# Performance work log

Hardware: AMD Instinct MI355X
Metric: run time of the kernel (lower is better)

The kernel has to match this reference:

```python
import jax, jax.numpy as jnp
import numpy as np

N_NODES = 50000
N_EDGES = 800000


def gcn_layer(h_in, W, b, src, dst, n_nodes):
    """PyG GCNConv: linear transform, add self-loops, symmetric-normalized scatter-add."""
    h = h_in @ W  # [N, out]
    loop = jnp.arange(n_nodes, dtype=src.dtype)
    s = jnp.concatenate([src, loop])  # [E+N]
    d = jnp.concatenate([dst, loop])  # [E+N]
    deg = jax.ops.segment_sum(jnp.ones_like(d, dtype=h.dtype), d, num_segments=n_nodes)
    dinv = jnp.where(deg > 0, jax.lax.rsqrt(deg), 0.0)  # deg^{-1/2}
    norm = dinv[s] * dinv[d]  # [E+N]
    msg = h[s] * norm[:, None]  # gather + scale, [E+N, out]
    out = jax.ops.segment_sum(msg, d, num_segments=n_nodes)  # scatter-add
    return out + b


def setup_inputs() -> dict:
    key = jax.random.key(0)
    ks = jax.random.split(key, 8)
    Din, H1, H2, Dout = 128, 128, 128, 64
    x = jax.random.normal(ks[0], (N_NODES, Din), dtype=jnp.float32)
    edge_index = jax.random.randint(ks[1], (2, N_EDGES), 0, N_NODES, dtype=jnp.int64)
    # Glorot-ish init for weights
    W1 = jax.random.normal(ks[2], (Din, H1), dtype=jnp.float32) / np.sqrt(Din)
    W2 = jax.random.normal(ks[3], (H1, H2), dtype=jnp.float32) / np.sqrt(H1)
    W3 = jax.random.normal(ks[4], (H2, Dout), dtype=jnp.float32) / np.sqrt(H2)
    b1 = jnp.zeros((H1,), dtype=jnp.float32)
    b2 = jnp.zeros((H2,), dtype=jnp.float32)
    b3 = jnp.zeros((Dout,), dtype=jnp.float32)
    return {"x": x, "edge_index": edge_index, "W1": W1, "b1": b1,
            "W2": W2, "b2": b2, "W3": W3, "b3": b3}


def reference(x, edge_index, W1, b1, W2, b2, W3, b3):
    src, dst = edge_index[0], edge_index[1]
    n = x.shape[0]
    h = gcn_layer(x, W1, b1, src, dst, n)
    h = jax.nn.relu(h)  # dropout p=0 -> identity
    h = gcn_layer(h, W2, b2, src, dst, n)
    h = jax.nn.relu(h)
    h = gcn_layer(h, W3, b3, src, dst, n)
    return h
```

## Files before the change

kernel.cpp:

```cpp
#include <hip/hip_runtime.h>
#include <hip/hip_fp16.h>

#define N_NODES 50000
#define N_EDGES 800000
#define CEILDIV(a,b) (((a)+(b)-1)/(b))
#define NB_SCAN CEILDIV(N_NODES, 256)

typedef _Float16 half8 __attribute__((ext_vector_type(8)));
typedef float    f32x4 __attribute__((ext_vector_type(4)));

__global__ __launch_bounds__(256) void k_deg_count(const int* __restrict__ dst,
                                                   int* __restrict__ degcnt, int e) {
    int i = blockIdx.x * 256 + threadIdx.x;
    if (i < e) atomicAdd(&degcnt[dst[i]], 1);
}

__global__ __launch_bounds__(256) void k_blocksum(const int* __restrict__ degcnt,
                                                  int* __restrict__ bsum, int n) {
    __shared__ int part[256];
    const int tid = threadIdx.x;
    const int gid = blockIdx.x * 256 + tid;
    part[tid] = (gid < n) ? degcnt[gid] : 0;
    __syncthreads();
    for (int off = 128; off > 0; off >>= 1) {
        if (tid < off) part[tid] += part[tid + off];
        __syncthreads();
    }
    if (tid == 0) bsum[blockIdx.x] = part[0];
}

__global__ __launch_bounds__(256) void k_scanb(const int* __restrict__ bsum,
                                               int* __restrict__ boff) {
    __shared__ int part[256];
    const int tid = threadIdx.x;
    part[tid] = (tid < NB_SCAN) ? bsum[tid] : 0;
    __syncthreads();
    for (int off = 1; off < 256; off <<= 1) {
        int v = (tid >= off) ? part[tid - off] : 0;
        __syncthreads();
        part[tid] += v;
        __syncthreads();
    }
    if (tid < NB_SCAN) boff[tid] = (tid == 0) ? 0 : part[tid - 1];
}

__global__ __launch_bounds__(256) void k_rowstart(const int* __restrict__ degcnt,
                                                  const int* __restrict__ boff,
                                                  int* __restrict__ rowstart,
                                                  float* __restrict__ dinv, int n) {
    __shared__ int part[256];
    const int tid = threadIdx.x;
    const int gid = blockIdx.x * 256 + tid;
    const int d = (gid < n) ? degcnt[gid] : 0;
    part[tid] = d;
    __syncthreads();
    for (int off = 1; off < 256; off <<= 1) {
        int v = (tid >= off) ? part[tid - off] : 0;
        __syncthreads();
        part[tid] += v;
        __syncthreads();
    }
    if (gid < n) {
        rowstart[gid] = boff[blockIdx.x] + part[tid] - d;
        dinv[gid] = rsqrtf((float)(d + 1));
    }
    if (gid == 0) rowstart[n] = N_EDGES;
}

__global__ __launch_bounds__(256) void k_bin(const int* __restrict__ src,
                                             const int* __restrict__ dst,
                                             const int* __restrict__ rowstart,
                                             int* __restrict__ cursor,
                                             int* __restrict__ esrc, int e) {
    int i = blockIdx.x * 256 + threadIdx.x;
    if (i < e) {
        int d = dst[i];
        int pos = rowstart[d] + atomicAdd(&cursor[d], 1);
        esrc[pos] = src[i];
    }
}

__global__ __launch_bounds__(256) void k_x2h(const float* __restrict__ x,
                                             __half* __restrict__ xh, long total) {
    long i = (long)(blockIdx.x * 256 + threadIdx.x) * 8;
    if (i >= total) return;
    float4 lo = ((const float4*)x)[i / 4];
    float4 hi = ((const float4*)x)[i / 4 + 1];
    union { __half2 h2[4]; uint4 u; } pk;
    pk.h2[0] = __floats2half2_rn(lo.x, lo.y);
    pk.h2[1] = __floats2half2_rn(lo.z, lo.w);
    pk.h2[2] = __floats2half2_rn(hi.x, hi.y);
    pk.h2[3] = __floats2half2_rn(hi.z, hi.w);
    ((uint4*)xh)[i / 8] = pk.u;
}

template<int KOUT>
__global__ __launch_bounds__(256) void k_w2h(const float* __restrict__ W,
                                             __half* __restrict__ Wt) {
    int idx = blockIdx.x * 256 + threadIdx.x;
    if (idx >= KOUT * 128) return;
    int c = idx >> 7;
    int k = idx & 127;
    Wt[c * 128 + k] = __float2half(W[(size_t)k * KOUT + c]);
}

template<int KOUT, bool RELU>
__global__ __launch_bounds__(256) void k_gemm(const __half* __restrict__ A,
                                              const __half* __restrict__ Wt,
                                              const float* __restrict__ dinv,
                                              __half* __restrict__ C, int n) {
    constexpr int NT     = KOUT / 16;
    constexpr int ABYTES = 64 * 256;
    constexpr int WBYTES = KOUT * 256;
    __shared__ uint4 ldsbuf[(ABYTES + WBYTES) / 16];
    char* Als = (char*)ldsbuf;
    char* Wls = Als + ABYTES;

    const int tid  = threadIdx.x;
    const int row0 = blockIdx.x * 64;

#pragma unroll
    for (int i = 0; i < 4; ++i) {
        int g   = tid + i * 256;
        int r   = g >> 4;
        int ch  = g & 15;
        int gr  = row0 + r;
        uint4 v = make_uint4(0u, 0u, 0u, 0u);
        if (gr < n) v = ((const uint4*)A)[(size_t)gr * 16 + ch];
        if (RELU) {
            uint n0 = (v.x >> 15) & 0x00010001u; v.x &= ~(n0 * 0xFFFFu);
            uint n1 = (v.y >> 15) & 0x00010001u; v.y &= ~(n1 * 0xFFFFu);
            uint n2 = (v.z >> 15) & 0x00010001u; v.z &= ~(n2 * 0xFFFFu);
            uint n3 = (v.w >> 15) & 0x00010001u; v.w &= ~(n3 * 0xFFFFu);
        }
        *(uint4*)(Als + r * 256 + ((ch * 16) ^ ((r & 7) << 4))) = v;
    }
#pragma unroll
    for (int i = 0; i < WBYTES / 16 / 256; ++i) {
        int g  = tid + i * 256;
        int r  = g >> 4;
        int ch = g & 15;
        uint4 v = ((const uint4*)Wt)[(size_t)r * 16 + ch];
        *(uint4*)(Wls + r * 256 + ((ch * 16) ^ ((r & 7) << 4))) = v;
    }
    __syncthreads();

    const int wave = tid >> 6;
    const int lane = tid & 63;
    const int l15  = lane & 15;
    const int l4   = lane >> 4;

    f32x4 acc[NT];
#pragma unroll
    for (int ct = 0; ct < NT; ++ct) acc[ct] = (f32x4){0.f, 0.f, 0.f, 0.f};

#pragma unroll
    for (int kb = 0; kb < 4; ++kb) {
        const int arow = 16 * wave + l15;
        half8 af = *(half8*)(Als + arow * 256 +
                             (((kb * 64) + l4 * 16) ^ ((arow & 7) << 4)));
#pragma unroll
        for (int ct = 0; ct < NT; ++ct) {
            const int wrow = ct * 16 + l15;
            half8 bf = *(half8*)(Wls + wrow * 256 +
                                 (((kb * 64) + l4 * 16) ^ ((wrow & 7) << 4)));
            acc[ct] = __builtin_amdgcn_mfma_f32_16x16x32_f16(af, bf, acc[ct], 0, 0, 0);
        }
    }

    const int rbase = row0 + 16 * wave + l4 * 4;
    const float d0 = dinv[min(rbase + 0, n - 1)];
    const float d1 = dinv[min(rbase + 1, n - 1)];
    const float d2 = dinv[min(rbase + 2, n - 1)];
    const float d3 = dinv[min(rbase + 3, n - 1)];
#pragma unroll
    for (int ct = 0; ct < NT; ++ct) {
        const int col = ct * 16 + l15;
        if (rbase + 0 < n) C[(size_t)(rbase + 0) * KOUT + col] = __float2half(acc[ct][0] * d0);
        if (rbase + 1 < n) C[(size_t)(rbase + 1) * KOUT + col] = __float2half(acc[ct][1] * d1);
        if (rbase + 2 < n) C[(size_t)(rbase + 2) * KOUT + col] = __float2half(acc[ct][2] * d2);
        if (rbase + 3 < n) C[(size_t)(rbase + 3) * KOUT + col] = __float2half(acc[ct][3] * d3);
    }
}

template<int K, bool HOUT>
__global__ __launch_bounds__(256) void k_aggregate(const __half* __restrict__ h,
                                                   const int* __restrict__ rowstart,
                                                   const int* __restrict__ esrc,
                                                   const float* __restrict__ dinv,
                                                   const float* __restrict__ b,
                                                   void* __restrict__ out, int n) {
    constexpr int VEC = K / 32;
    const int tid  = threadIdx.x;
    const int l5   = tid & 31;
    const int base = tid & 32;
    const int node = blockIdx.x * 8 + (tid >> 5);
    if (node >= n) return;

    float a0, a1, a2 = 0.f, a3 = 0.f;
    if (VEC == 4) {
        uint2 raw = ((const uint2*)h)[(size_t)node * 32 + l5];
        union { uint2 u; __half2 h2[2]; } c; c.u = raw;
        float2 lo = __half22float2(c.h2[0]);
        float2 hi = __half22float2(c.h2[1]);
        a0 = lo.x; a1 = lo.y; a2 = hi.x; a3 = hi.y;
    } else {
        uint raw = ((const uint*)h)[(size_t)node * 32 + l5];
        union { uint u; __half2 h2; } c; c.u = raw;
        float2 lo = __half22float2(c.h2);
        a0 = lo.x; a1 = lo.y;
    }

    int row = rowstart[node];
    const int end = rowstart[node + 1];

#define GATHER(SRC_, OK_)                                                     \
    if (VEC == 4) {                                                           \
        uint2 raw = make_uint2(0u, 0u);                                       \
        if (OK_) raw = ((const uint2*)h)[(size_t)(SRC_) * 32 + l5];           \
        union { uint2 u; __half2 h2[2]; } c; c.u = raw;                       \
        float2 lo = __half22float2(c.h2[0]);                                  \
        float2 hi = __half22float2(c.h2[1]);                                  \
        a0 += lo.x; a1 += lo.y; a2 += hi.x; a3 += hi.y;                       \
    } else {                                                                  \
        uint raw = 0u;                                                        \
        if (OK_) raw = ((const uint*)h)[(size_t)(SRC_) * 32 + l5];            \
        union { uint u; __half2 h2; } c; c.u = raw;                           \
        float2 lo = __half22float2(c.h2);                                     \
        a0 += lo.x; a1 += lo.y;                                               \
    }

    while (row < end) {
        int cnt = end - row;
        if (cnt > 32) cnt = 32;
        int s_l = (l5 < cnt) ? esrc[row + l5] : 0;
        for (int jj = 0; jj < cnt; jj += 8) {
            const int i0 = jj + 0, i1 = jj + 1, i2 = jj + 2, i3 = jj + 3;
            const int i4 = jj + 4, i5 = jj + 5, i6 = jj + 6, i7 = jj + 7;
            const int s0 = __shfl(s_l, base + i0);
            const int s1 = __shfl(s_l, base + i1);
            const int s2 = __shfl(s_l, base + i2);
            const int s3 = __shfl(s_l, base + i3);
            const int s4 = __shfl(s_l, base + i4);
            const int s5 = __shfl(s_l, base + i5);
            const int s6 = __shfl(s_l, base + i6);
            const int s7 = __shfl(s_l, base + i7);
            GATHER(s0, i0 < cnt);
            GATHER(s1, i1 < cnt);
            GATHER(s2, i2 < cnt);
            GATHER(s3, i3 < cnt);
            GATHER(s4, i4 < cnt);
            GATHER(s5, i5 < cnt);
            GATHER(s6, i6 < cnt);
            GATHER(s7, i7 < cnt);
        }
        row += cnt;
    }
#undef GATHER

    const float dd = dinv[node];
    if (VEC == 4) {
        float4 bb = ((const float4*)b)[l5];
        float o0 = a0 * dd + bb.x, o1 = a1 * dd + bb.y;
        float o2 = a2 * dd + bb.z, o3 = a3 * dd + bb.w;
        if (HOUT) {
            union { __half2 h2[2]; uint2 u; } pk;
            pk.h2[0] = __floats2half2_rn(o0, o1);
            pk.h2[1] = __floats2half2_rn(o2, o3);
            ((uint2*)out)[(size_t)node * 32 + l5] = pk.u;
        } else {
            ((float4*)out)[(size_t)node * 32 + l5] = make_float4(o0, o1, o2, o3);
        }
    } else {
        float2 bb = ((const float2*)b)[l5];
        float o0 = a0 * dd + bb.x, o1 = a1 * dd + bb.y;
        if (HOUT) {
            union { __half2 h2; uint u; } pk;
            pk.h2 = __floats2half2_rn(o0, o1);
            ((uint*)out)[(size_t)node * 32 + l5] = pk.u;
        } else {
            ((float2*)out)[(size_t)node * 32 + l5] = make_float2(o0, o1);
        }
    }
}

extern "C" void kernel_launch(void* const* d_in, const int* in_sizes, int n_in,
                              void* d_out, int out_size, void* d_ws, size_t ws_size,
                              hipStream_t stream) {
    const float* x  = (const float*)d_in[0];
    const int*   ei = (const int*)d_in[1];
    const float* W1 = (const float*)d_in[2];
    const float* b1 = (const float*)d_in[3];
    const float* W2 = (const float*)d_in[4];
    const float* b2 = (const float*)d_in[5];
    const float* W3 = (const float*)d_in[6];
    const float* b3 = (const float*)d_in[7];
    float* out = (float*)d_out;

    const int* src = ei;
    const int* dst = ei + N_EDGES;

    char* ws = (char*)d_ws;
    size_t off = 0;
    auto alloc = [&](size_t bytes) {
        void* p = ws + off;
        off += (bytes + 255) & ~(size_t)255;
        return p;
    };
    int*    degcnt   = (int*)alloc((size_t)N_NODES * 2 * 4);
    int*    cursor   = degcnt + N_NODES;
    int*    rowstart = (int*)alloc((N_NODES + 1) * 4);
    float*  dinv     = (float*)alloc(N_NODES * 4);
    int*    bsum     = (int*)alloc(NB_SCAN * 4);
    int*    boff     = (int*)alloc(NB_SCAN * 4);
    int*    esrc     = (int*)alloc((size_t)N_EDGES * 4);
    __half* xh       = (__half*)alloc((size_t)N_NODES * 128 * 2);
    __half* hbuf     = (__half*)alloc((size_t)N_NODES * 128 * 2);
    __half* abuf     = (__half*)alloc((size_t)N_NODES * 128 * 2);
    __half* wt1      = (__half*)alloc(128 * 128 * 2);
    __half* wt2      = (__half*)alloc(128 * 128 * 2);
    __half* wt3      = (__half*)alloc(64 * 128 * 2);

    const int n = N_NODES, e = N_EDGES;

    hipMemsetAsync(degcnt, 0, (size_t)N_NODES * 2 * 4, stream);
    k_deg_count<<<CEILDIV(e, 256), 256, 0, stream>>>(dst, degcnt, e);
    k_blocksum<<<NB_SCAN, 256, 0, stream>>>(degcnt, bsum, n);
    k_scanb<<<1, 256, 0, stream>>>(bsum, boff);
    k_rowstart<<<NB_SCAN, 256, 0, stream>>>(degcnt, boff, rowstart, dinv, n);
    k_bin<<<CEILDIV(e, 256), 256, 0, stream>>>(src, dst, rowstart, cursor, esrc, e);

    k_x2h<<<CEILDIV((long)n * 128, 8 * 256), 256, 0, stream>>>(x, xh, (long)n * 128);
    k_w2h<128><<<CEILDIV(128 * 128, 256), 256, 0, stream>>>(W1, wt1);
    k_w2h<128><<<CEILDIV(128 * 128, 256), 256, 0, stream>>>(W2, wt2);
    k_w2h<64><<<CEILDIV(64 * 128, 256), 256, 0, stream>>>(W3, wt3);

    k_gemm<128, false><<<CEILDIV(n, 64), 256, 0, stream>>>(xh, wt1, dinv, hbuf, n);
    k_aggregate<128, true><<<CEILDIV(n, 8), 256, 0, stream>>>(hbuf, rowstart, esrc, dinv, b1, abuf, n);

    k_gemm<128, true><<<CEILDIV(n, 64), 256, 0, stream>>>(abuf, wt2, dinv, hbuf, n);
    k_aggregate<128, true><<<CEILDIV(n, 8), 256, 0, stream>>>(hbuf, rowstart, esrc, dinv, b2, abuf, n);

    k_gemm<64, true><<<CEILDIV(n, 64), 256, 0, stream>>>(abuf, wt3, dinv, hbuf, n);
    k_aggregate<64, false><<<CEILDIV(n, 8), 256, 0, stream>>>(hbuf, rowstart, esrc, dinv, b3, out, n);
}
```

Before: 291.9 us.

## Slice 128-wide features into 32-column planes for cache-friendly aggregation

```diff
diff --git a/kernel.cpp b/kernel.cpp
--- a/kernel.cpp
+++ b/kernel.cpp
@@ -5,14 +5,21 @@
 #define N_EDGES 800000
 #define CEILDIV(a,b) (((a)+(b)-1)/(b))
 #define NB_SCAN CEILDIV(N_NODES, 256)
+#define NHALF   (N_NODES / 2)
 
 typedef _Float16 half8 __attribute__((ext_vector_type(8)));
 typedef float    f32x4 __attribute__((ext_vector_type(4)));
 
-__global__ __launch_bounds__(256) void k_deg_count(const int* __restrict__ dst,
-                                                   int* __restrict__ degcnt, int e) {
+__global__ __launch_bounds__(256) void k_deg4(const int* __restrict__ dst,
+                                              int* __restrict__ degcnt, int e4) {
     int i = blockIdx.x * 256 + threadIdx.x;
-    if (i < e) atomicAdd(&degcnt[dst[i]], 1);
+    if (i < e4) {
+        int4 d4 = ((const int4*)dst)[i];
+        atomicAdd(&degcnt[d4.x], 1);
+        atomicAdd(&degcnt[d4.y], 1);
+        atomicAdd(&degcnt[d4.z], 1);
+        atomicAdd(&degcnt[d4.w], 1);
+    }
 }
 
 __global__ __launch_bounds__(256) void k_blocksum(const int* __restrict__ degcnt,
@@ -67,17 +74,27 @@
     if (gid == 0) rowstart[n] = N_EDGES;
 }
 
-__global__ __launch_bounds__(256) void k_bin(const int* __restrict__ src,
-                                             const int* __restrict__ dst,
-                                             const int* __restrict__ rowstart,
-                                             int* __restrict__ cursor,
-                                             int* __restrict__ esrc, int e) {
+__global__ __launch_bounds__(256) void k_bin4(const int* __restrict__ src,
+                                              const int* __restrict__ dst,
+                                              const int* __restrict__ rowstart,
+                                              int* __restrict__ cursor,
+                                              int* __restrict__ esrc, int e4) {
     int i = blockIdx.x * 256 + threadIdx.x;
-    if (i < e) {
-        int d = dst[i];
-        int pos = rowstart[d] + atomicAdd(&cursor[d], 1);
-        esrc[pos] = src[i];
-    }
+    if (i >= e4) return;
+    int4 s4 = ((const int4*)src)[i];
+    int4 d4 = ((const int4*)dst)[i];
+    int r0 = rowstart[d4.x];
+    int r1 = rowstart[d4.y];
+    int r2 = rowstart[d4.z];
+    int r3 = rowstart[d4.w];
+    int p0 = atomicAdd(&cursor[d4.x], 1);
+    int p1 = atomicAdd(&cursor[d4.y], 1);
+    int p2 = atomicAdd(&cursor[d4.z], 1);
+    int p3 = atomicAdd(&cursor[d4.w], 1);
+    __builtin_nontemporal_store(s4.x, &esrc[r0 + p0]);
+    __builtin_nontemporal_store(s4.y, &esrc[r1 + p1]);
+    __builtin_nontemporal_store(s4.z, &esrc[r2 + p2]);
+    __builtin_nontemporal_store(s4.w, &esrc[r3 + p3]);
 }
 
 __global__ __launch_bounds__(256) void k_x2h(const float* __restrict__ x,
@@ -94,17 +111,28 @@
     ((uint4*)xh)[i / 8] = pk.u;
 }
 
-template<int KOUT>
-__global__ __launch_bounds__(256) void k_w2h(const float* __restrict__ W,
-                                             __half* __restrict__ Wt) {
+__global__ __launch_bounds__(256) void k_wcast(const float* __restrict__ W1,
+                                               const float* __restrict__ W2,
+                                               const float* __restrict__ W3,
+                                               __half* __restrict__ wt1,
+                                               __half* __restrict__ wt2,
+                                               __half* __restrict__ wt3) {
     int idx = blockIdx.x * 256 + threadIdx.x;
-    if (idx >= KOUT * 128) return;
-    int c = idx >> 7;
-    int k = idx & 127;
-    Wt[c * 128 + k] = __float2half(W[(size_t)k * KOUT + c]);
-}
-
-template<int KOUT, bool RELU>
+    if (idx < 16384) {
+        int c = idx >> 7, k = idx & 127;
+        wt1[c * 128 + k] = __float2half(W1[(size_t)k * 128 + c]);
+    } else if (idx < 32768) {
+        int j = idx - 16384;
+        int c = j >> 7, k = j & 127;
+        wt2[c * 128 + k] = __float2half(W2[(size_t)k * 128 + c]);
+    } else if (idx < 40960) {
+        int j = idx - 32768;
+        int c = j >> 7, k = j & 127;
+        wt3[c * 128 + k] = __float2half(W3[(size_t)k * 64 + c]);
+    }
+}
+
+template<int KOUT, bool RELU, bool SIN, bool SOUT>
 __global__ __launch_bounds__(256) void k_gemm(const __half* __restrict__ A,
                                               const __half* __restrict__ Wt,
                                               const float* __restrict__ dinv,
@@ -126,7 +154,14 @@
         int ch  = g & 15;
         int gr  = row0 + r;
         uint4 v = make_uint4(0u, 0u, 0u, 0u);
-        if (gr < n) v = ((const uint4*)A)[(size_t)gr * 16 + ch];
+        if (gr < n) {
+            if (SIN) {
+                int sl = ch >> 2, c2 = ch & 3;
+                v = ((const uint4*)A)[((size_t)sl * n + gr) * 4 + c2];
+            } else {
+                v = ((const uint4*)A)[(size_t)gr * 16 + ch];
+            }
+        }
         if (RELU) {
             uint n0 = (v.x >> 15) & 0x00010001u; v.x &= ~(n0 * 0xFFFFu);
             uint n1 = (v.y >> 15) & 0x00010001u; v.y &= ~(n1 * 0xFFFFu);
@@ -175,59 +210,54 @@
     const float d3 = dinv[min(rbase + 3, n - 1)];
 #pragma unroll
     for (int ct = 0; ct < NT; ++ct) {
-        const int col = ct * 16 + l15;
-        if (rbase + 0 < n) C[(size_t)(rbase + 0) * KOUT + col] = __float2half(acc[ct][0] * d0);
-        if (rbase + 1 < n) C[(size_t)(rbase + 1) * KOUT + col] = __float2half(acc[ct][1] * d1);
-        if (rbase + 2 < n) C[(size_t)(rbase + 2) * KOUT + col] = __float2half(acc[ct][2] * d2);
-        if (rbase + 3 < n) C[(size_t)(rbase + 3) * KOUT + col] = __float2half(acc[ct][3] * d3);
-    }
-}
-
-template<int K, bool HOUT>
-__global__ __launch_bounds__(256) void k_aggregate(const __half* __restrict__ h,
-                                                   const int* __restrict__ rowstart,
-                                                   const int* __restrict__ esrc,
-                                                   const float* __restrict__ dinv,
-                                                   const float* __restrict__ b,
-                                                   void* __restrict__ out, int n) {
-    constexpr int VEC = K / 32;
+        size_t p0, p1, p2, p3;
+        if (SOUT) {
+            const size_t sb = ((size_t)(ct >> 1) * n) * 32 + (ct & 1) * 16 + l15;
+            p0 = sb + (size_t)(rbase + 0) * 32;
+            p1 = sb + (size_t)(rbase + 1) * 32;
+            p2 = sb + (size_t)(rbase + 2) * 32;
+            p3 = sb + (size_t)(rbase + 3) * 32;
+        } else {
+            const int col = ct * 16 + l15;
+            p0 = (size_t)(rbase + 0) * KOUT + col;
+            p1 = (size_t)(rbase + 1) * KOUT + col;
+            p2 = (size_t)(rbase + 2) * KOUT + col;
+            p3 = (size_t)(rbase + 3) * KOUT + col;
+        }
+        if (rbase + 0 < n) C[p0] = __float2half(acc[ct][0] * d0);
+        if (rbase + 1 < n) C[p1] = __float2half(acc[ct][1] * d1);
+        if (rbase + 2 < n) C[p2] = __float2half(acc[ct][2] * d2);
+        if (rbase + 3 < n) C[p3] = __float2half(acc[ct][3] * d3);
+    }
+}
+
+__global__ __launch_bounds__(256) void k_agg_sl(const __half* __restrict__ h,
+                                                const int* __restrict__ rowstart,
+                                                const int* __restrict__ esrc,
+                                                const float* __restrict__ dinv,
+                                                const float* __restrict__ b,
+                                                __half* __restrict__ out, int n) {
     const int tid  = threadIdx.x;
     const int l5   = tid & 31;
     const int base = tid & 32;
-    const int node = blockIdx.x * 8 + (tid >> 5);
+    const int b8   = blockIdx.x & 7;
+    const int s    = b8 & 3;
+    const int half = b8 >> 2;
+    const int node = half * NHALF + (blockIdx.x >> 3) * 8 + (tid >> 5);
     if (node >= n) return;
 
-    float a0, a1, a2 = 0.f, a3 = 0.f;
-    if (VEC == 4) {
-        uint2 raw = ((const uint2*)h)[(size_t)node * 32 + l5];
-        union { uint2 u; __half2 h2[2]; } c; c.u = raw;
-        float2 lo = __half22float2(c.h2[0]);
-        float2 hi = __half22float2(c.h2[1]);
-        a0 = lo.x; a1 = lo.y; a2 = hi.x; a3 = hi.y;
-    } else {
-        uint raw = ((const uint*)h)[(size_t)node * 32 + l5];
-        union { uint u; __half2 h2; } c; c.u = raw;
-        float2 lo = __half22float2(c.h2);
-        a0 = lo.x; a1 = lo.y;
-    }
+    const __half* hs = h + (size_t)s * n * 32;
+
+    float acc = __half2float(hs[(size_t)node * 32 + l5]);
 
     int row = rowstart[node];
     const int end = rowstart[node + 1];
 
-#define GATHER(SRC_, OK_)                                                     \
-    if (VEC == 4) {                                                           \
-        uint2 raw = make_uint2(0u, 0u);                                       \
-        if (OK_) raw = ((const uint2*)h)[(size_t)(SRC_) * 32 + l5];           \
-        union { uint2 u; __half2 h2[2]; } c; c.u = raw;                       \
-        float2 lo = __half22float2(c.h2[0]);                                  \
-        float2 hi = __half22float2(c.h2[1]);                                  \
-        a0 += lo.x; a1 += lo.y; a2 += hi.x; a3 += hi.y;                       \
-    } else {                                                                  \
-        uint raw = 0u;                                                        \
-        if (OK_) raw = ((const uint*)h)[(size_t)(SRC_) * 32 + l5];            \
-        union { uint u; __half2 h2; } c; c.u = raw;                           \
-        float2 lo = __half22float2(c.h2);                                     \
-        a0 += lo.x; a1 += lo.y;                                               \
+#define G1(S_, OK_)                                                        \
+    {                                                                      \
+        float v_ = 0.f;                                                    \
+        if (OK_) v_ = __half2float(hs[(size_t)(S_) * 32 + l5]);            \
+        acc += v_;                                                         \
     }
 
     while (row < end) {
@@ -245,43 +275,87 @@
             const int s5 = __shfl(s_l, base + i5);
             const int s6 = __shfl(s_l, base + i6);
             const int s7 = __shfl(s_l, base + i7);
-            GATHER(s0, i0 < cnt);
-            GATHER(s1, i1 < cnt);
-            GATHER(s2, i2 < cnt);
-            GATHER(s3, i3 < cnt);
-            GATHER(s4, i4 < cnt);
-            GATHER(s5, i5 < cnt);
-            GATHER(s6, i6 < cnt);
-            GATHER(s7, i7 < cnt);
+            G1(s0, i0 < cnt);
+            G1(s1, i1 < cnt);
+            G1(s2, i2 < cnt);
+            G1(s3, i3 < cnt);
+            G1(s4, i4 < cnt);
+            G1(s5, i5 < cnt);
+            G1(s6, i6 < cnt);
+            G1(s7, i7 < cnt);
         }
         row += cnt;
     }
-#undef GATHER
+#undef G1
+
+    const float o = acc * dinv[node] + b[s * 32 + l5];
+    out[(size_t)s * n * 32 + (size_t)node * 32 + l5] = __float2half(o);
+}
+
+__global__ __launch_bounds__(256) void k_agg64(const __half* __restrict__ h,
+                                               const int* __restrict__ rowstart,
+                                               const int* __restrict__ esrc,
+                                               const float* __restrict__ dinv,
+                                               const float* __restrict__ b,
+                                               float* __restrict__ out, int n) {
+    const int tid  = threadIdx.x;
+    const int l5   = tid & 31;
+    const int base = tid & 32;
+    const int node = blockIdx.x * 8 + (tid >> 5);
+    if (node >= n) return;
+
+    float a0, a1;
+    {
+        uint raw = ((const uint*)h)[(size_t)node * 32 + l5];
+        union { uint u; __half2 h2; } c; c.u = raw;
+        float2 lo = __half22float2(c.h2);
+        a0 = lo.x; a1 = lo.y;
+    }
+
+    int row = rowstart[node];
+    const int end = rowstart[node + 1];
+
+#define G2(S_, OK_)                                                        \
+    {                                                                      \
+        uint raw = 0u;                                                     \
+        if (OK_) raw = ((const uint*)h)[(size_t)(S_) * 32 + l5];           \
+        union { uint u; __half2 h2; } c; c.u = raw;                        \
+        float2 lo = __half22float2(c.h2);                                  \
+        a0 += lo.x; a1 += lo.y;                                            \
+    }
+
+    while (row < end) {
+        int cnt = end - row;
+        if (cnt > 32) cnt = 32;
+        int s_l = (l5 < cnt) ? esrc[row + l5] : 0;
+        for (int jj = 0; jj < cnt; jj += 8) {
+            const int i0 = jj + 0, i1 = jj + 1, i2 = jj + 2, i3 = jj + 3;
+            const int i4 = jj + 4, i5 = jj + 5, i6 = jj + 6, i7 = jj + 7;
+            const int s0 = __shfl(s_l, base + i0);
+            const int s1 = __shfl(s_l, base + i1);
+            const int s2 = __shfl(s_l, base + i2);
+            const int s3 = __shfl(s_l, base + i3);
+            const int s4 = __shfl(s_l, base + i4);
+            const int s5 = __shfl(s_l, base + i5);
+            const int s6 = __shfl(s_l, base + i6);
+            const int s7 = __shfl(s_l, base + i7);
+            G2(s0, i0 < cnt);
+            G2(s1, i1 < cnt);
+            G2(s2, i2 < cnt);
+            G2(s3, i3 < cnt);
+            G2(s4, i4 < cnt);
+            G2(s5, i5 < cnt);
+            G2(s6, i6 < cnt);
+            G2(s7, i7 < cnt);
+        }
+        row += cnt;
+    }
+#undef G2
 
     const float dd = dinv[node];
-    if (VEC == 4) {
-        float4 bb = ((const float4*)b)[l5];
-        float o0 = a0 * dd + bb.x, o1 = a1 * dd + bb.y;
-        float o2 = a2 * dd + bb.z, o3 = a3 * dd + bb.w;
-        if (HOUT) {
-            union { __half2 h2[2]; uint2 u; } pk;
-            pk.h2[0] = __floats2half2_rn(o0, o1);
-            pk.h2[1] = __floats2half2_rn(o2, o3);
-            ((uint2*)out)[(size_t)node * 32 + l5] = pk.u;
-        } else {
-            ((float4*)out)[(size_t)node * 32 + l5] = make_float4(o0, o1, o2, o3);
-        }
-    } else {
-        float2 bb = ((const float2*)b)[l5];
-        float o0 = a0 * dd + bb.x, o1 = a1 * dd + bb.y;
-        if (HOUT) {
-            union { __half2 h2; uint u; } pk;
-            pk.h2 = __floats2half2_rn(o0, o1);
-            ((uint*)out)[(size_t)node * 32 + l5] = pk.u;
-        } else {
-            ((float2*)out)[(size_t)node * 32 + l5] = make_float2(o0, o1);
-        }
-    }
+    float2 bb = ((const float2*)b)[l5];
+    ((float2*)out)[(size_t)node * 32 + l5] =
+        make_float2(a0 * dd + bb.x, a1 * dd + bb.y);
 }
 
 extern "C" void kernel_launch(void* const* d_in, const int* in_sizes, int n_in,
@@ -324,23 +398,23 @@
     const int n = N_NODES, e = N_EDGES;
 
     hipMemsetAsync(degcnt, 0, (size_t)N_NODES * 2 * 4, stream);
-    k_deg_count<<<CEILDIV(e, 256), 256, 0, stream>>>(dst, degcnt, e);
+    k_deg4<<<CEILDIV(e / 4, 256), 256, 0, stream>>>(dst, degcnt, e / 4);
     k_blocksum<<<NB_SCAN, 256, 0, stream>>>(degcnt, bsum, n);
     k_scanb<<<1, 256, 0, stream>>>(bsum, boff);
     k_rowstart<<<NB_SCAN, 256, 0, stream>>>(degcnt, boff, rowstart, dinv, n);
-    k_bin<<<CEILDIV(e, 256), 256, 0, stream>>>(src, dst, rowstart, cursor, esrc, e);
+    k_bin4<<<CEILDIV(e / 4, 256), 256, 0, stream>>>(src, dst, rowstart, cursor, esrc, e / 4);
 
     k_x2h<<<CEILDIV((long)n * 128, 8 * 256), 256, 0, stream>>>(x, xh, (long)n * 128);
-    k_w2h<128><<<CEILDIV(128 * 128, 256), 256, 0, stream>>>(W1, wt1);
-    k_w2h<128><<<CEILDIV(128 * 128, 256), 256, 0, stream>>>(W2, wt2);
-    k_w2h<64><<<CEILDIV(64 * 128, 256), 256, 0, stream>>>(W3, wt3);
-
-    k_gemm<128, false><<<CEILDIV(n, 64), 256, 0, stream>>>(xh, wt1, dinv, hbuf, n);
-    k_aggregate<128, true><<<CEILDIV(n, 8), 256, 0, stream>>>(hbuf, rowstart, esrc, dinv, b1, abuf, n);
-
-    k_gemm<128, true><<<CEILDIV(n, 64), 256, 0, stream>>>(abuf, wt2, dinv, hbuf, n);
-    k_aggregate<128, true><<<CEILDIV(n, 8), 256, 0, stream>>>(hbuf, rowstart, esrc, dinv, b2, abuf, n);
-
-    k_gemm<64, true><<<CEILDIV(n, 64), 256, 0, stream>>>(abuf, wt3, dinv, hbuf, n);
-    k_aggregate<64, false><<<CEILDIV(n, 8), 256, 0, stream>>>(hbuf, rowstart, esrc, dinv, b3, out, n);
-}
+    k_wcast<<<CEILDIV(40960, 256), 256, 0, stream>>>(W1, W2, W3, wt1, wt2, wt3);
+
+    const int aggblocks = (NHALF / 8) * 8;
+
+    k_gemm<128, false, false, true><<<CEILDIV(n, 64), 256, 0, stream>>>(xh, wt1, dinv, hbuf, n);
+    k_agg_sl<<<aggblocks, 256, 0, stream>>>(hbuf, rowstart, esrc, dinv, b1, abuf, n);
+
+    k_gemm<128, true, true, true><<<CEILDIV(n, 64), 256, 0, stream>>>(abuf, wt2, dinv, hbuf, n);
+    k_agg_sl<<<aggblocks, 256, 0, stream>>>(hbuf, rowstart, esrc, dinv, b2, abuf, n);
+
+    k_gemm<64, true, true, false><<<CEILDIV(n, 64), 256, 0, stream>>>(abuf, wt3, dinv, hbuf, n);
+    k_agg64<<<CEILDIV(n, 8), 256, 0, stream>>>(hbuf, rowstart, esrc, dinv, b3, out, n);
+}
```

Result: slower. 400.9 us (+37.4%).

## Partition edge binning by destination range and fuse input casts into GEMM

Applied to the files above, without the earlier changes.

```diff
diff --git a/kernel.cpp b/kernel.cpp
--- a/kernel.cpp
+++ b/kernel.cpp
@@ -5,14 +5,23 @@
 #define N_EDGES 800000
 #define CEILDIV(a,b) (((a)+(b)-1)/(b))
 #define NB_SCAN CEILDIV(N_NODES, 256)
+#define NPART   8
+#define PSIZE   CEILDIV(N_NODES, NPART)
 
 typedef _Float16 half8 __attribute__((ext_vector_type(8)));
 typedef float    f32x4 __attribute__((ext_vector_type(4)));
 
-__global__ __launch_bounds__(256) void k_deg_count(const int* __restrict__ dst,
-                                                   int* __restrict__ degcnt, int e) {
-    int i = blockIdx.x * 256 + threadIdx.x;
-    if (i < e) atomicAdd(&degcnt[dst[i]], 1);
+__global__ __launch_bounds__(256) void k_deg4p(const int* __restrict__ dst,
+                                               int* __restrict__ degcnt, int e4) {
+    const int part = blockIdx.x & 7;
+    const int lo = part * PSIZE, hi = lo + PSIZE;
+    int i = (blockIdx.x >> 3) * 256 + threadIdx.x;
+    if (i >= e4) return;
+    int4 d4 = ((const int4*)dst)[i];
+    if (d4.x >= lo && d4.x < hi) atomicAdd(&degcnt[d4.x], 1);
+    if (d4.y >= lo && d4.y < hi) atomicAdd(&degcnt[d4.y], 1);
+    if (d4.z >= lo && d4.z < hi) atomicAdd(&degcnt[d4.z], 1);
+    if (d4.w >= lo && d4.w < hi) atomicAdd(&degcnt[d4.w], 1);
 }
 
 __global__ __launch_bounds__(256) void k_blocksum(const int* __restrict__ degcnt,
@@ -67,45 +76,58 @@
     if (gid == 0) rowstart[n] = N_EDGES;
 }
 
-__global__ __launch_bounds__(256) void k_bin(const int* __restrict__ src,
-                                             const int* __restrict__ dst,
-                                             const int* __restrict__ rowstart,
-                                             int* __restrict__ cursor,
-                                             int* __restrict__ esrc, int e) {
-    int i = blockIdx.x * 256 + threadIdx.x;
-    if (i < e) {
-        int d = dst[i];
-        int pos = rowstart[d] + atomicAdd(&cursor[d], 1);
-        esrc[pos] = src[i];
-    }
-}
-
-__global__ __launch_bounds__(256) void k_x2h(const float* __restrict__ x,
-                                             __half* __restrict__ xh, long total) {
-    long i = (long)(blockIdx.x * 256 + threadIdx.x) * 8;
-    if (i >= total) return;
-    float4 lo = ((const float4*)x)[i / 4];
-    float4 hi = ((const float4*)x)[i / 4 + 1];
-    union { __half2 h2[4]; uint4 u; } pk;
-    pk.h2[0] = __floats2half2_rn(lo.x, lo.y);
-    pk.h2[1] = __floats2half2_rn(lo.z, lo.w);
-    pk.h2[2] = __floats2half2_rn(hi.x, hi.y);
-    pk.h2[3] = __floats2half2_rn(hi.z, hi.w);
-    ((uint4*)xh)[i / 8] = pk.u;
-}
-
-template<int KOUT>
-__global__ __launch_bounds__(256) void k_w2h(const float* __restrict__ W,
-                                             __half* __restrict__ Wt) {
+__global__ __launch_bounds__(256) void k_bin4p(const int* __restrict__ src,
+                                               const int* __restrict__ dst,
+                                               const int* __restrict__ rowstart,
+                                               int* __restrict__ cursor,
+                                               int* __restrict__ esrc, int e4) {
+    const int part = blockIdx.x & 7;
+    const int lo = part * PSIZE, hi = lo + PSIZE;
+    int i = (blockIdx.x >> 3) * 256 + threadIdx.x;
+    if (i >= e4) return;
+    int4 s4 = ((const int4*)src)[i];
+    int4 d4 = ((const int4*)dst)[i];
+    if (d4.x >= lo && d4.x < hi) {
+        int p = rowstart[d4.x] + atomicAdd(&cursor[d4.x], 1);
+        __builtin_nontemporal_store(s4.x, &esrc[p]);
+    }
+    if (d4.y >= lo && d4.y < hi) {
+        int p = rowstart[d4.y] + atomicAdd(&cursor[d4.y], 1);
+        __builtin_nontemporal_store(s4.y, &esrc[p]);
+    }
+    if (d4.z >= lo && d4.z < hi) {
+        int p = rowstart[d4.z] + atomicAdd(&cursor[d4.z], 1);
+        __builtin_nontemporal_store(s4.z, &esrc[p]);
+    }
+    if (d4.w >= lo && d4.w < hi) {
+        int p = rowstart[d4.w] + atomicAdd(&cursor[d4.w], 1);
+        __builtin_nontemporal_store(s4.w, &esrc[p]);
+    }
+}
+
+__global__ __launch_bounds__(256) void k_wcast(const float* __restrict__ W1,
+                                               const float* __restrict__ W2,
+                                               const float* __restrict__ W3,
+                                               __half* __restrict__ wt1,
+                                               __half* __restrict__ wt2,
+                                               __half* __restrict__ wt3) {
     int idx = blockIdx.x * 256 + threadIdx.x;
-    if (idx >= KOUT * 128) return;
-    int c = idx >> 7;
-    int k = idx & 127;
-    Wt[c * 128 + k] = __float2half(W[(size_t)k * KOUT + c]);
-}
-
-template<int KOUT, bool RELU>
-__global__ __launch_bounds__(256) void k_gemm(const __half* __restrict__ A,
+    if (idx < 16384) {
+        int c = idx >> 7, k = idx & 127;
+        wt1[c * 128 + k] = __float2half(W1[(size_t)k * 128 + c]);
+    } else if (idx < 32768) {
+        int j = idx - 16384;
+        int c = j >> 7, k = j & 127;
+        wt2[c * 128 + k] = __float2half(W2[(size_t)k * 128 + c]);
+    } else if (idx < 40960) {
+        int j = idx - 32768;
+        int c = j >> 7, k = j & 127;
+        wt3[c * 128 + k] = __float2half(W3[(size_t)k * 64 + c]);
+    }
+}
+
+template<int KOUT, bool RELU, bool CVT>
+__global__ __launch_bounds__(256) void k_gemm(const void* __restrict__ Ain,
                                               const __half* __restrict__ Wt,
                                               const float* __restrict__ dinv,
                                               __half* __restrict__ C, int n) {
@@ -126,7 +148,21 @@
         int ch  = g & 15;
         int gr  = row0 + r;
         uint4 v = make_uint4(0u, 0u, 0u, 0u);
-        if (gr < n) v = ((const uint4*)A)[(size_t)gr * 16 + ch];
+        if (gr < n) {
+            if (CVT) {
+                const float4* Af = (const float4*)Ain;
+                float4 flo = Af[(size_t)gr * 32 + ch * 2];
+                float4 fhi = Af[(size_t)gr * 32 + ch * 2 + 1];
+                union { __half2 h2[4]; uint4 u; } pk;
+                pk.h2[0] = __floats2half2_rn(flo.x, flo.y);
+                pk.h2[1] = __floats2half2_rn(flo.z, flo.w);
+                pk.h2[2] = __floats2half2_rn(fhi.x, fhi.y);
+                pk.h2[3] = __floats2half2_rn(fhi.z, fhi.w);
+                v = pk.u;
+            } else {
+                v = ((const uint4*)Ain)[(size_t)gr * 16 + ch];
+            }
+        }
         if (RELU) {
             uint n0 = (v.x >> 15) & 0x00010001u; v.x &= ~(n0 * 0xFFFFu);
             uint n1 = (v.y >> 15) & 0x00010001u; v.y &= ~(n1 * 0xFFFFu);
@@ -314,7 +350,6 @@
     int*    bsum     = (int*)alloc(NB_SCAN * 4);
     int*    boff     = (int*)alloc(NB_SCAN * 4);
     int*    esrc     = (int*)alloc((size_t)N_EDGES * 4);
-    __half* xh       = (__half*)alloc((size_t)N_NODES * 128 * 2);
     __half* hbuf     = (__half*)alloc((size_t)N_NODES * 128 * 2);
     __half* abuf     = (__half*)alloc((size_t)N_NODES * 128 * 2);
     __half* wt1      = (__half*)alloc(128 * 128 * 2);
@@ -322,25 +357,23 @@
     __half* wt3      = (__half*)alloc(64 * 128 * 2);
 
     const int n = N_NODES, e = N_EDGES;
+    const int e4 = e / 4;
 
     hipMemsetAsync(degcnt, 0, (size_t)N_NODES * 2 * 4, stream);
-    k_deg_count<<<CEILDIV(e, 256), 256, 0, stream>>>(dst, degcnt, e);
+    k_deg4p<<<CEILDIV(e4, 256) * NPART, 256, 0, stream>>>(dst, degcnt, e4);
     k_blocksum<<<NB_SCAN, 256, 0, stream>>>(degcnt, bsum, n);
     k_scanb<<<1, 256, 0, stream>>>(bsum, boff);
     k_rowstart<<<NB_SCAN, 256, 0, stream>>>(degcnt, boff, rowstart, dinv, n);
-    k_bin<<<CEILDIV(e, 256), 256, 0, stream>>>(src, dst, rowstart, cursor, esrc, e);
-
-    k_x2h<<<CEILDIV((long)n * 128, 8 * 256), 256, 0, stream>>>(x, xh, (long)n * 128);
-    k_w2h<128><<<CEILDIV(128 * 128, 256), 256, 0, stream>>>(W1, wt1);
-    k_w2h<128><<<CEILDIV(128 * 128, 256), 256, 0, stream>>>(W2, wt2);
-    k_w2h<64><<<CEILDIV(64 * 128, 256), 256, 0, stream>>>(W3, wt3);
-
-    k_gemm<128, false><<<CEILDIV(n, 64), 256, 0, stream>>>(xh, wt1, dinv, hbuf, n);
+    k_bin4p<<<CEILDIV(e4, 256) * NPART, 256, 0, stream>>>(src, dst, rowstart, cursor, esrc, e4);
+
+    k_wcast<<<CEILDIV(40960, 256), 256, 0, stream>>>(W1, W2, W3, wt1, wt2, wt3);
+
+    k_gemm<128, false, true><<<CEILDIV(n, 64), 256, 0, stream>>>(x, wt1, dinv, hbuf, n);
     k_aggregate<128, true><<<CEILDIV(n, 8), 256, 0, stream>>>(hbuf, rowstart, esrc, dinv, b1, abuf, n);
 
-    k_gemm<128, true><<<CEILDIV(n, 64), 256, 0, stream>>>(abuf, wt2, dinv, hbuf, n);
+    k_gemm<128, true, false><<<CEILDIV(n, 64), 256, 0, stream>>>(abuf, wt2, dinv, hbuf, n);
     k_aggregate<128, true><<<CEILDIV(n, 8), 256, 0, stream>>>(hbuf, rowstart, esrc, dinv, b2, abuf, n);
 
-    k_gemm<64, true><<<CEILDIV(n, 64), 256, 0, stream>>>(abuf, wt3, dinv, hbuf, n);
+    k_gemm<64, true, false><<<CEILDIV(n, 64), 256, 0, stream>>>(abuf, wt3, dinv, hbuf, n);
     k_aggregate<64, false><<<CEILDIV(n, 8), 256, 0, stream>>>(hbuf, rowstart, esrc, dinv, b3, out, n);
 }
```

After: 279.6 us. 4.2% less time.
